# Kernel optimization log

Hardware: AMD Instinct MI355X
Metric: run time of the kernel (lower is better)

The kernel has to match this reference:

```python
import jax, jax.numpy as jnp
import numpy as np

PRE_NMS = 256       # pre_nms_limit default
IOU_THRESH = 0.7    # iou_threshold default
POST_NMS = 128      # post_nms_limit default


def setup_inputs() -> dict:
    key = jax.random.key(0)
    ks = jax.random.split(key, 8)
    B, N, D = 16, 2048, 1024
    feats = jax.random.normal(ks[0], (B, N, D), dtype=jnp.float32)
    # valid boxes in (x1, y1, x2, y2) format
    xy1 = jax.random.uniform(ks[1], (B, N, 2), dtype=jnp.float32) * 1000.0
    wh = jax.random.uniform(ks[2], (B, N, 2), dtype=jnp.float32) * 200.0 + 1.0
    proposals = jnp.concatenate([xy1, xy1 + wh], axis=-1)
    def lin(k, fi, fo):
        return jax.random.normal(k, (fi, fo), dtype=jnp.float32) * (1.0 / np.sqrt(fi))
    Ws1 = lin(ks[3], D, 256); bs1 = jnp.zeros((256,), jnp.float32)
    Ws2 = lin(ks[4], 256, 64); bs2 = jnp.zeros((64,), jnp.float32)
    Wo1 = lin(ks[5], D, 256); bo1 = jnp.zeros((256,), jnp.float32)
    Wo2 = lin(ks[6], 256, 64); bo2 = jnp.zeros((64,), jnp.float32)
    return dict(feats=feats, proposals=proposals, Ws1=Ws1, bs1=bs1, Ws2=Ws2,
                bs2=bs2, Wo1=Wo1, bo1=bo1, Wo2=Wo2, bo2=bo2)


def _nms_keep(boxes, thresh):
    """Greedy NMS; boxes (P,4) already sorted by descending score."""
    P = boxes.shape[0]
    areas = (boxes[:, 2] - boxes[:, 0]) * (boxes[:, 3] - boxes[:, 1])
    lt = jnp.maximum(boxes[:, None, :2], boxes[None, :, :2])
    rb = jnp.minimum(boxes[:, None, 2:], boxes[None, :, 2:])
    wh = jnp.clip(rb - lt, 0.0)
    inter = wh[..., 0] * wh[..., 1]
    iou = inter / (areas[:, None] + areas[None, :] - inter)
    idx = jnp.arange(P)
    def body(i, keep):
        suppress = (iou[i] > thresh) & (idx > i) & keep[i]
        return keep & ~suppress
    return jax.lax.fori_loop(0, P, body, jnp.ones((P,), bool))


def _image_forward(f, boxes, Ws1, bs1, Ws2, bs2, Wo1, bo1, Wo2, bo2):
    # RelPNSimilarity: two small MLPs + sigmoid(subj @ obj^T)
    subj = jax.nn.relu(f @ Ws1 + bs1) @ Ws2 + bs2        # (N, 64)
    obj = jax.nn.relu(f @ Wo1 + bo1) @ Wo2 + bo2         # (N, 64)
    scores = jax.nn.sigmoid(subj @ obj.T)                # (N, N)
    N = f.shape[0]
    # full descending sort + take == top_k; flat index f = i*N + j -> pair (i, j)
    top_scores, top_idx = jax.lax.top_k(scores.reshape(-1), PRE_NMS)
    si = top_idx // N
    oi = top_idx % N
    pairs = jnp.stack([si, oi], axis=1)                  # (PRE_NMS, 2)
    b1 = boxes[si]
    b2 = boxes[oi]
    inter_boxes = jnp.concatenate(
        [jnp.maximum(b1[:, :2], b2[:, :2]), jnp.minimum(b1[:, 2:], b2[:, 2:])],
        axis=1)                                          # (PRE_NMS, 4)
    keep = _nms_keep(inter_boxes, IOU_THRESH)
    # kept indices in score order, padded with non-kept if fewer than POST_NMS
    P = PRE_NMS
    order = jnp.argsort(jnp.where(keep, jnp.arange(P), P + jnp.arange(P)))
    sel = order[:POST_NMS]
    valid = keep[sel]
    out_pairs = jnp.where(valid[:, None], pairs[sel], 0)
    out_scores = jnp.where(valid, top_scores[sel], 0.0)
    out_inter = jnp.where(valid[:, None], inter_boxes[sel], 0.0)
    return out_pairs, out_scores, out_inter, valid


def reference(feats, proposals, Ws1, bs1, Ws2, bs2, Wo1, bo1, Wo2, bo2):
    fn = jax.vmap(_image_forward,
                  in_axes=(0, 0, None, None, None, None, None, None, None, None))
    pairs, scores, inters, valid = fn(feats, proposals, Ws1, bs1, Ws2, bs2,
                                      Wo1, bo1, Wo2, bo2)
    # pairs (B,128,2) int, scores (B,128), inters (B,128,4), valid (B,128) bool
    return pairs, scores, inters, valid
```

## Files before the change

kernel.cpp:

```cpp
#include <hip/hip_runtime.h>
#include <stdint.h>


#define N_PROP 2048
#define D_FEAT 1024
#define H_DIM  256
#define E_DIM  64
#define BATCH  16
#define PRE_NMS 256
#define POST_NMS 128
#define CAND_CAP 32768
#define CNT_STRIDE 64
#define LOGIT_THRESH 11.0f
#define IOU_T 0.7f
#define WT_WHICH (16 * 32 * 512)
#define SO_ELEMS ((size_t)BATCH * 128 * 2 * 512)
#define LBUF_CAP 2048

typedef short sh8 __attribute__((ext_vector_type(8)));
typedef float f4  __attribute__((ext_vector_type(4)));

__device__ inline void decomp3(float f, unsigned& h, unsigned& m, unsigned& l) {
    unsigned u = __float_as_uint(f);
    h = (u + 0x8000u) & 0xFFFF0000u;
    float f1 = f - __uint_as_float(h);
    unsigned u1 = __float_as_uint(f1);
    m = (u1 + 0x8000u) & 0xFFFF0000u;
    float f2 = f1 - __uint_as_float(m);
    l = (__float_as_uint(f2) + 0x8000u) & 0xFFFF0000u;
}

__global__ __launch_bounds__(256) void prep_kernel(
    const float* __restrict__ Ws1, const float* __restrict__ Wo1,
    unsigned short* __restrict__ Wh, unsigned short* __restrict__ Wm,
    unsigned short* __restrict__ Wl)
{
    const int t = threadIdx.x;
    const int nblk = blockIdx.x;
    const int ks = blockIdx.y * 4 + (t >> 6);
    const int which = blockIdx.z;
    const float* W = which ? Wo1 : Ws1;
    const int lane = t & 63;
    const int q = lane >> 4, ln = lane & 15;

    unsigned hb[8], mb[8], lb[8];
#pragma unroll
    for (int j = 0; j < 8; ++j) {
        float v = W[(size_t)(ks * 32 + q * 8 + j) * H_DIM + nblk * 16 + ln];
        decomp3(v, hb[j], mb[j], lb[j]);
    }
    union { unsigned u[4]; sh8 v; } H, M, L;
#pragma unroll
    for (int c = 0; c < 4; ++c) {
        H.u[c] = (hb[2 * c] >> 16) | (hb[2 * c + 1] & 0xFFFF0000u);
        M.u[c] = (mb[2 * c] >> 16) | (mb[2 * c + 1] & 0xFFFF0000u);
        L.u[c] = (lb[2 * c] >> 16) | (lb[2 * c + 1] & 0xFFFF0000u);
    }
    size_t off = ((size_t)which * 16 * 32 + (size_t)nblk * 32 + ks) * 512 + lane * 8;
    *(sh8*)(Wh + off) = H.v;
    *(sh8*)(Wm + off) = M.v;
    *(sh8*)(Wl + off) = L.v;
}

__global__ __launch_bounds__(256) void mlp_fused_kernel(
    const float* __restrict__ feats,
    const unsigned short* __restrict__ Wh, const unsigned short* __restrict__ Wm,
    const unsigned short* __restrict__ Wl,
    const float* __restrict__ bs1,
    const float* __restrict__ Ws2, const float* __restrict__ bs2,
    const float* __restrict__ bo1,
    const float* __restrict__ Wo2, const float* __restrict__ bo2,
    unsigned short* __restrict__ Sh, unsigned short* __restrict__ Sm,
    unsigned short* __restrict__ Sl,
    unsigned short* __restrict__ Oh, unsigned short* __restrict__ Om,
    unsigned short* __restrict__ Ol)
{
    const int t  = threadIdx.x;
    const int rt = blockIdx.x;
    const int b  = blockIdx.y;
    const int r0g = rt * 32;

    __shared__ float lds[4128];
    float* Fs = lds;

    const int lane = t & 63;
    const int l15 = t & 15;
    const int q   = (t >> 4) & 3;
    const int wv  = t >> 6;
    const int wb  = wv * 64;

    f4 acc[2][2][4];
#pragma unroll
    for (int w = 0; w < 2; ++w)
#pragma unroll
        for (int i = 0; i < 2; ++i)
#pragma unroll
            for (int j = 0; j < 4; ++j) acc[w][i][j] = (f4)0.0f;

    const float* fbase = feats + ((size_t)b * N_PROP + r0g) * D_FEAT;
    const int fm = t >> 3, fj = t & 7;

    float4 fpre = *(const float4*)(fbase + (size_t)fm * D_FEAT + fj * 4);

    sh8 nxh[2], nxm[2], nxl[2];
#pragma unroll
    for (int w = 0; w < 2; ++w) {
        size_t off = (size_t)w * WT_WHICH + ((size_t)(wv * 4) * 32) * 512 + lane * 8;
        nxh[w] = *(const sh8*)(Wh + off);
        nxm[w] = *(const sh8*)(Wm + off);
        nxl[w] = *(const sh8*)(Wl + off);
    }

    for (int kt = 0; kt < 32; ++kt) {
        __syncthreads();
        *(float4*)(Fs + fm * 36 + fj * 4) = fpre;
        __syncthreads();
        if (kt + 1 < 32)
            fpre = *(const float4*)(fbase + (size_t)fm * D_FEAT + (kt + 1) * 32 + fj * 4);

        sh8 afh[2], afm[2], afl[2];
#pragma unroll
        for (int mt = 0; mt < 2; ++mt) {
            const float* src = Fs + (mt * 16 + l15) * 36 + q * 8;
            float4 a0 = *(const float4*)(src);
            float4 a1 = *(const float4*)(src + 4);
            float av[8] = {a0.x, a0.y, a0.z, a0.w, a1.x, a1.y, a1.z, a1.w};
            unsigned hb[8], mb[8], lb[8];
#pragma unroll
            for (int e = 0; e < 8; ++e) decomp3(av[e], hb[e], mb[e], lb[e]);
            union { unsigned u[4]; sh8 v; } H, M, L;
#pragma unroll
            for (int c = 0; c < 4; ++c) {
                H.u[c] = (hb[2 * c] >> 16) | (hb[2 * c + 1] & 0xFFFF0000u);
                M.u[c] = (mb[2 * c] >> 16) | (mb[2 * c + 1] & 0xFFFF0000u);
                L.u[c] = (lb[2 * c] >> 16) | (lb[2 * c + 1] & 0xFFFF0000u);
            }
            afh[mt] = H.v; afm[mt] = M.v; afl[mt] = L.v;
        }

#pragma unroll
        for (int nt = 0; nt < 4; ++nt) {
            sh8 cwh[2], cwm[2], cwl[2];
#pragma unroll
            for (int w = 0; w < 2; ++w) {
                cwh[w] = nxh[w]; cwm[w] = nxm[w]; cwl[w] = nxl[w];
            }
            int s = kt * 4 + nt + 1;
            if (s < 128) {
                int knt = s & 3, kkt = s >> 2;
#pragma unroll
                for (int w = 0; w < 2; ++w) {
                    size_t off = (size_t)w * WT_WHICH
                               + ((size_t)(wv * 4 + knt) * 32 + kkt) * 512 + lane * 8;
                    nxh[w] = *(const sh8*)(Wh + off);
                    nxm[w] = *(const sh8*)(Wm + off);
                    nxl[w] = *(const sh8*)(Wl + off);
                }
            }
#pragma unroll
            for (int w = 0; w < 2; ++w)
#pragma unroll
                for (int mt = 0; mt < 2; ++mt) {
                    f4 x = acc[w][mt][nt];
                    x = __builtin_amdgcn_mfma_f32_16x16x32_bf16(afh[mt], cwh[w], x, 0, 0, 0);
                    x = __builtin_amdgcn_mfma_f32_16x16x32_bf16(afh[mt], cwm[w], x, 0, 0, 0);
                    x = __builtin_amdgcn_mfma_f32_16x16x32_bf16(afm[mt], cwh[w], x, 0, 0, 0);
                    x = __builtin_amdgcn_mfma_f32_16x16x32_bf16(afh[mt], cwl[w], x, 0, 0, 0);
                    x = __builtin_amdgcn_mfma_f32_16x16x32_bf16(afm[mt], cwm[w], x, 0, 0, 0);
                    x = __builtin_amdgcn_mfma_f32_16x16x32_bf16(afl[mt], cwh[w], x, 0, 0, 0);
                    acc[w][mt][nt] = x;
                }
        }
    }

    float bc[2][4];
#pragma unroll
    for (int w = 0; w < 2; ++w) {
        const float* B1 = w ? bo1 : bs1;
#pragma unroll
        for (int nt = 0; nt < 4; ++nt) bc[w][nt] = B1[wb + nt * 16 + l15];
    }

    float* Hp  = lds;
    float* W2c = lds + 2080;
    const int tr2 = t >> 4;
    const int tc2 = t & 15;

#pragma unroll
    for (int w = 0; w < 2; ++w) {
        const float* W2 = w ? Wo2 : Ws2;
        const float* B2 = w ? bo2 : bs2;
        unsigned short* Dh = w ? Oh : Sh;
        unsigned short* Dm = w ? Om : Sm;
        unsigned short* Dl = w ? Ol : Sl;

        float acc2[2][4];
#pragma unroll
        for (int i = 0; i < 2; ++i)
#pragma unroll
            for (int j = 0; j < 4; ++j) acc2[i][j] = 0.0f;

        float4 w2pre[2];
#pragma unroll
        for (int i = 0; i < 2; ++i) {
            int lin = (t + i * 256) * 4;
            int row = lin >> 6, col = lin & 63;
            w2pre[i] = *(const float4*)(W2 + (size_t)row * E_DIM + col);
        }

        for (int c = 0; c < 8; ++c) {
            const int p = c >> 1, ch = c & 1;
            __syncthreads();
            if (ch == 0 && wv == p) {
#pragma unroll
                for (int mt = 0; mt < 2; ++mt)
#pragma unroll
                    for (int nt = 0; nt < 4; ++nt)
#pragma unroll
                        for (int r = 0; r < 4; ++r) {
                            float v = acc[w][mt][nt][r] + bc[w][nt];
                            v = v > 0.0f ? v : 0.0f;
                            Hp[(mt * 16 + q * 4 + r) * 65 + nt * 16 + l15] = v;
                        }
            }
#pragma unroll
            for (int i = 0; i < 2; ++i) {
                int lin = (t + i * 256) * 4;
                int row = lin >> 6, col = lin & 63;
                *(float4*)(W2c + row * 64 + col) = w2pre[i];
            }
            if (c + 1 < 8) {
                const int rbase = (c + 1) * 32;
#pragma unroll
                for (int i = 0; i < 2; ++i) {
                    int lin = (t + i * 256) * 4;
                    int row = lin >> 6, col = lin & 63;
                    w2pre[i] = *(const float4*)(W2 + (size_t)(rbase + row) * E_DIM + col);
                }
            }
            __syncthreads();
#pragma unroll 8
            for (int kk = 0; kk < 32; ++kk) {
                int kl = ch * 32 + kk;
                float4 wvv = *(const float4*)(W2c + kk * 64 + tc2 * 4);
                float hv[2];
#pragma unroll
                for (int ri = 0; ri < 2; ++ri) hv[ri] = Hp[(tr2 * 2 + ri) * 65 + kl];
#pragma unroll
                for (int ri = 0; ri < 2; ++ri) {
                    acc2[ri][0] = fmaf(hv[ri], wvv.x, acc2[ri][0]);
                    acc2[ri][1] = fmaf(hv[ri], wvv.y, acc2[ri][1]);
                    acc2[ri][2] = fmaf(hv[ri], wvv.z, acc2[ri][2]);
                    acc2[ri][3] = fmaf(hv[ri], wvv.w, acc2[ri][3]);
                }
            }
        }

        {
            float bb[4] = {B2[tc2 * 4 + 0], B2[tc2 * 4 + 1],
                           B2[tc2 * 4 + 2], B2[tc2 * 4 + 3]};
            const int ks = tc2 >> 3, q2 = (tc2 >> 1) & 3, j0 = (tc2 & 1) * 4;
#pragma unroll
            for (int ri = 0; ri < 2; ++ri) {
                unsigned hb[4], mb[4], lb[4];
#pragma unroll
                for (int ci = 0; ci < 4; ++ci)
                    decomp3(acc2[ri][ci] + bb[ci], hb[ci], mb[ci], lb[ci]);
                int row = r0g + tr2 * 2 + ri;
                int nblk = row >> 4, ln = row & 15;
                size_t so = (((size_t)b * 128 + nblk) * 2 + ks) * 512
                            + (q2 * 16 + ln) * 8 + j0;
                *(uint2*)(Dh + so) = make_uint2((hb[0] >> 16) | (hb[1] & 0xFFFF0000u),
                                                (hb[2] >> 16) | (hb[3] & 0xFFFF0000u));
                *(uint2*)(Dm + so) = make_uint2((mb[0] >> 16) | (mb[1] & 0xFFFF0000u),
                                                (mb[2] >> 16) | (mb[3] & 0xFFFF0000u));
                *(uint2*)(Dl + so) = make_uint2((lb[0] >> 16) | (lb[1] & 0xFFFF0000u),
                                                (lb[2] >> 16) | (lb[3] & 0xFFFF0000u));
            }
        }
    }
}

__global__ __launch_bounds__(256) void score_kernel(
    const unsigned short* __restrict__ Sh, const unsigned short* __restrict__ Sm,
    const unsigned short* __restrict__ Sl,
    const unsigned short* __restrict__ Oh, const unsigned short* __restrict__ Om,
    const unsigned short* __restrict__ Ol,
    unsigned long long* __restrict__ cand, unsigned int* __restrict__ cnt)
{
    const int t = threadIdx.x;
    const int lane = t & 63;
    const int wv = t >> 6;
    const int rt = blockIdx.x >> 1;
    const int half = blockIdx.x & 1;
    const int b = blockIdx.y;
    const int r0g = rt * 64;
    const int ct0 = half * 16, ctEnd = ct0 + 16;
    const int l15 = t & 15;
    const int q   = (t >> 4) & 3;
    const int rh  = wv & 1;
    const int chh = wv >> 1;

    __shared__ unsigned long long lbuf[LBUF_CAP];
    __shared__ unsigned int lcnt, nOut, gbase;
    if (t == 0) lcnt = 0;
    __syncthreads();

    sh8 sfh[2][2], sfm[2][2], sfl[2][2];
#pragma unroll
    for (int mt = 0; mt < 2; ++mt)
#pragma unroll
        for (int ks = 0; ks < 2; ++ks) {
            size_t off = (((size_t)b * 128 + rt * 4 + rh * 2 + mt) * 2 + ks) * 512
                         + lane * 8;
            sfh[mt][ks] = *(const sh8*)(Sh + off);
            sfm[mt][ks] = *(const sh8*)(Sm + off);
            sfl[mt][ks] = *(const sh8*)(Sl + off);
        }

    sh8 oAh[2][2], oAm[2][2], oAl[2][2];
    sh8 oBh[2][2], oBm[2][2], oBl[2][2];

    auto load_o = [&](sh8 (&oh)[2][2], sh8 (&om)[2][2], sh8 (&ol)[2][2], int ct) {
        if (ct < ctEnd) {
#pragma unroll
            for (int nt = 0; nt < 2; ++nt)
#pragma unroll
                for (int ks = 0; ks < 2; ++ks) {
                    size_t off = (((size_t)b * 128 + ct * 4 + chh * 2 + nt) * 2 + ks) * 512
                                 + lane * 8;
                    oh[nt][ks] = *(const sh8*)(Oh + off);
                    om[nt][ks] = *(const sh8*)(Om + off);
                    ol[nt][ks] = *(const sh8*)(Ol + off);
                }
        }
    };

    auto compute = [&](sh8 (&oh)[2][2], sh8 (&om)[2][2], sh8 (&ol)[2][2], int ct) {
        f4 acc[2][2];
#pragma unroll
        for (int mt = 0; mt < 2; ++mt)
#pragma unroll
            for (int nt = 0; nt < 2; ++nt) {
                f4 x = (f4)0.0f;
#pragma unroll
                for (int ks = 0; ks < 2; ++ks) {
                    x = __builtin_amdgcn_mfma_f32_16x16x32_bf16(sfh[mt][ks], oh[nt][ks], x, 0, 0, 0);
                    x = __builtin_amdgcn_mfma_f32_16x16x32_bf16(sfh[mt][ks], om[nt][ks], x, 0, 0, 0);
                    x = __builtin_amdgcn_mfma_f32_16x16x32_bf16(sfm[mt][ks], oh[nt][ks], x, 0, 0, 0);
                    x = __builtin_amdgcn_mfma_f32_16x16x32_bf16(sfh[mt][ks], ol[nt][ks], x, 0, 0, 0);
                    x = __builtin_amdgcn_mfma_f32_16x16x32_bf16(sfm[mt][ks], om[nt][ks], x, 0, 0, 0);
                    x = __builtin_amdgcn_mfma_f32_16x16x32_bf16(sfl[mt][ks], oh[nt][ks], x, 0, 0, 0);
                }
                acc[mt][nt] = x;
            }
#pragma unroll
        for (int mt = 0; mt < 2; ++mt)
#pragma unroll
            for (int nt = 0; nt < 2; ++nt)
#pragma unroll
                for (int r = 0; r < 4; ++r) {
                    float logit = acc[mt][nt][r];
                    if (logit > LOGIT_THRESH) {
                        float score = 1.0f / (1.0f + expf(-logit));
                        unsigned sb = __float_as_uint(score);
                        int row = r0g + rh * 32 + mt * 16 + q * 4 + r;
                        int col = ct * 64 + chh * 32 + nt * 16 + l15;
                        unsigned flat = (unsigned)(row * N_PROP + col);
                        unsigned long long key =
                            ((unsigned long long)sb << 32) | (unsigned)(~flat);
                        unsigned p = atomicAdd(&lcnt, 1u);
                        if (p < LBUF_CAP) lbuf[p] = key;
                    }
                }
    };

    load_o(oAh, oAm, oAl, ct0);
    for (int i = 0; i < 16; i += 2) {
        load_o(oBh, oBm, oBl, ct0 + i + 1);
        compute(oAh, oAm, oAl, ct0 + i);
        load_o(oAh, oAm, oAl, ct0 + i + 2);
        compute(oBh, oBm, oBl, ct0 + i + 1);
    }

    __syncthreads();
    if (t == 0) {
        unsigned n = lcnt > LBUF_CAP ? LBUF_CAP : lcnt;
        nOut = n;
        gbase = n ? atomicAdd(&cnt[(size_t)b * CNT_STRIDE], n) : 0u;
    }
    __syncthreads();
    for (unsigned i = t; i < nOut; i += 256) {
        unsigned pos = gbase + i;
        if (pos < CAND_CAP) cand[(size_t)b * CAND_CAP + pos] = lbuf[i];
    }
}

__device__ inline void bitonic_sort_desc_u64(unsigned long long* a, unsigned n, int t) {
    for (unsigned k = 2; k <= n; k <<= 1)
        for (unsigned j = k >> 1; j > 0; j >>= 1) {
            __syncthreads();
            for (unsigned i = (unsigned)t; i < n; i += 256) {
                unsigned l = i ^ j;
                if (l > i) {
                    unsigned long long x = a[i], y = a[l];
                    bool up = ((i & k) == 0);
                    if (up ? (x < y) : (x > y)) { a[i] = y; a[l] = x; }
                }
            }
        }
    __syncthreads();
}

__global__ __launch_bounds__(256) void select_nms_kernel(
    const unsigned long long* __restrict__ cand, const unsigned int* __restrict__ cnt,
    const float* __restrict__ proposals, float* __restrict__ out)
{
    const int b = blockIdx.x;
    const int t = threadIdx.x;
    const int lane = t & 63;
    const int wv = t >> 6;
    __shared__ unsigned int hist[1024];
    __shared__ unsigned long long selk[256];
    __shared__ unsigned long long pool[4096];
    __shared__ unsigned int nDef, nPool, kc_s, need_s;
    __shared__ float bx1[256], by1[256], bx2[256], by2[256], barea[256];
    __shared__ unsigned int keepf[256];
    __shared__ unsigned int wcnt[4];

    unsigned count = cnt[(size_t)b * CNT_STRIDE];
    if (count > CAND_CAP) count = CAND_CAP;

    for (int i = t; i < 1024; i += 256) hist[i] = 0;
    selk[t] = 0ull;
    if (t == 0) { nDef = 0; nPool = 0; }
    __syncthreads();

    const unsigned long long* cb = cand + (size_t)b * CAND_CAP;
    for (unsigned i = t; i < count; i += 256) {
        unsigned k = 0x3F800000u - (unsigned)(cb[i] >> 32);
        if (k > 1023u) k = 1023u;
        atomicAdd(&hist[k], 1u);
    }
    __syncthreads();
    if (t == 0) {
        unsigned c = 0, kc = 1024, need = 0;
        for (int k = 0; k < 1024; ++k) {
            unsigned prev = c;
            c += hist[k];
            if (c >= PRE_NMS) { kc = (unsigned)k; need = PRE_NMS - prev; break; }
        }
        kc_s = kc; need_s = need;
    }
    __syncthreads();
    const unsigned kc = kc_s, need = need_s;

    for (unsigned i = t; i < count; i += 256) {
        unsigned long long key = cb[i];
        unsigned k = 0x3F800000u - (unsigned)(key >> 32);
        if (k > 1023u) k = 1023u;
        if (k < kc) {
            unsigned p = atomicAdd(&nDef, 1u);
            if (p < 256u) selk[p] = key;
        } else if (k == kc) {
            unsigned p = atomicAdd(&nPool, 1u);
            if (p < 4096u) pool[p] = key;
        }
    }
    __syncthreads();
    unsigned np = nPool; if (np > 4096u) np = 4096u;
    unsigned n2 = 256; while (n2 < np) n2 <<= 1;
    for (unsigned i = t; i < n2; i += 256) if (i >= np) pool[i] = 0ull;
    __syncthreads();
    bitonic_sort_desc_u64(pool, n2, t);

    unsigned nd = nDef; if (nd > 256u) nd = 256u;
    if ((unsigned)t < need && nd + (unsigned)t < 256u) selk[nd + t] = pool[t];
    __syncthreads();
    bitonic_sort_desc_u64(selk, 256u, t);

    float rx1, ry1, rx2, ry2, rar, rscore;
    int rsi, roi;
    {
        unsigned long long key = selk[t];
        unsigned flat = ~(unsigned)(key & 0xFFFFFFFFull);
        unsigned si = (flat >> 11) & 2047u;
        unsigned oi = flat & 2047u;
        rscore = __uint_as_float((unsigned)(key >> 32));
        const float* p1 = proposals + ((size_t)b * N_PROP + si) * 4;
        const float* p2 = proposals + ((size_t)b * N_PROP + oi) * 4;
        rx1 = fmaxf(p1[0], p2[0]);
        ry1 = fmaxf(p1[1], p2[1]);
        rx2 = fminf(p1[2], p2[2]);
        ry2 = fminf(p1[3], p2[3]);
        rar = (rx2 - rx1) * (ry2 - ry1);
        bx1[t] = rx1; by1[t] = ry1; bx2[t] = rx2; by2[t] = ry2; barea[t] = rar;
        rsi = (int)si; roi = (int)oi;
    }
    __syncthreads();

    bool kreg = true;
    for (int w = 0; w < 4; ++w) {
        if (wv == w) {
            for (int l = 0; l < 64; ++l) {
                int   ki  = __shfl((int)kreg, l);
                float ix1 = __shfl(rx1, l);
                float iy1 = __shfl(ry1, l);
                float ix2 = __shfl(rx2, l);
                float iy2 = __shfl(ry2, l);
                float iar = __shfl(rar, l);
                if (ki && lane > l) {
                    float lx = fmaxf(ix1, rx1), ly = fmaxf(iy1, ry1);
                    float rx = fminf(ix2, rx2), ry = fminf(iy2, ry2);
                    float wd = rx - lx; if (wd < 0.0f) wd = 0.0f;
                    float ht = ry - ly; if (ht < 0.0f) ht = 0.0f;
                    float inter = wd * ht;
                    float iou = inter / (iar + rar - inter);
                    if (iou > IOU_T) kreg = false;
                }
            }
            keepf[t] = kreg ? 1u : 0u;
        }
        __syncthreads();
        if (wv > w) {
            for (int l = 0; l < 64; ++l) {
                int i = w * 64 + l;
                if (keepf[i]) {
                    float lx = fmaxf(bx1[i], rx1), ly = fmaxf(by1[i], ry1);
                    float rx = fminf(bx2[i], rx2), ry = fminf(by2[i], ry2);
                    float wd = rx - lx; if (wd < 0.0f) wd = 0.0f;
                    float ht = ry - ly; if (ht < 0.0f) ht = 0.0f;
                    float inter = wd * ht;
                    float iou = inter / (barea[i] + rar - inter);
                    if (iou > IOU_T) kreg = false;
                }
            }
        }
    }
    __syncthreads();

    unsigned long long m = __ballot(kreg);
    unsigned before = __popcll(m & ((1ull << lane) - 1ull));
    if (lane == 0) wcnt[wv] = (unsigned)__popcll(m);
    __syncthreads();
    unsigned base = 0, tot = 0;
#pragma unroll
    for (int w = 0; w < 4; ++w) {
        unsigned c = wcnt[w];
        if (w < wv) base += c;
        tot += c;
    }
    unsigned kb = base + before;
    unsigned pos = kreg ? kb : (tot + (unsigned)t - kb);
    if (pos < POST_NMS) {
        bool valid = kreg;
        float* pairs = out;
        float* scr = out + (size_t)BATCH * POST_NMS * 2;
        float* itb = scr + (size_t)BATCH * POST_NMS;
        float* vld = itb + (size_t)BATCH * POST_NMS * 4;
        size_t s = (size_t)b * POST_NMS + pos;
        pairs[s * 2 + 0] = valid ? (float)rsi : 0.0f;
        pairs[s * 2 + 1] = valid ? (float)roi : 0.0f;
        scr[s] = valid ? rscore : 0.0f;
        itb[s * 4 + 0] = valid ? rx1 : 0.0f;
        itb[s * 4 + 1] = valid ? ry1 : 0.0f;
        itb[s * 4 + 2] = valid ? rx2 : 0.0f;
        itb[s * 4 + 3] = valid ? ry2 : 0.0f;
        vld[s] = valid ? 1.0f : 0.0f;
    }
}

extern "C" void kernel_launch(void* const* d_in, const int* in_sizes, int n_in,
                              void* d_out, int out_size, void* d_ws, size_t ws_size,
                              hipStream_t stream) {
    const float* feats     = (const float*)d_in[0];
    const float* proposals = (const float*)d_in[1];
    const float* Ws1 = (const float*)d_in[2];
    const float* bs1 = (const float*)d_in[3];
    const float* Ws2 = (const float*)d_in[4];
    const float* bs2 = (const float*)d_in[5];
    const float* Wo1 = (const float*)d_in[6];
    const float* bo1 = (const float*)d_in[7];
    const float* Wo2 = (const float*)d_in[8];
    const float* bo2 = (const float*)d_in[9];
    float* out = (float*)d_out;

    char* ws = (char*)d_ws;
    unsigned long long* cand = (unsigned long long*)ws;
    unsigned int* cnt = (unsigned int*)(cand + (size_t)BATCH * CAND_CAP);
    unsigned short* Wth = (unsigned short*)(cnt + BATCH * CNT_STRIDE);
    unsigned short* Wtm = Wth + 2 * WT_WHICH;
    unsigned short* Wtl = Wtm + 2 * WT_WHICH;
    unsigned short* Sh = Wtl + 2 * WT_WHICH;
    unsigned short* Sm = Sh + SO_ELEMS;
    unsigned short* Sl = Sm + SO_ELEMS;
    unsigned short* Oh = Sl + SO_ELEMS;
    unsigned short* Om = Oh + SO_ELEMS;
    unsigned short* Ol = Om + SO_ELEMS;

    hipMemsetAsync(cnt, 0, BATCH * CNT_STRIDE * sizeof(unsigned int), stream);

    prep_kernel<<<dim3(16, 8, 2), 256, 0, stream>>>(Ws1, Wo1, Wth, Wtm, Wtl);
    mlp_fused_kernel<<<dim3(64, BATCH), 256, 0, stream>>>(
        feats, Wth, Wtm, Wtl, bs1, Ws2, bs2, bo1, Wo2, bo2,
        Sh, Sm, Sl, Oh, Om, Ol);
    score_kernel<<<dim3(64, BATCH), 256, 0, stream>>>(
        Sh, Sm, Sl, Oh, Om, Ol, cand, cnt);
    select_nms_kernel<<<BATCH, 256, 0, stream>>>(cand, cnt, proposals, out);
}
```

Before: 592.0 us.

## Split features into bf16 parts once per tile and share object tiles via LDS

Result: slower. 625.6 us (+5.7%).

```diff
diff --git a/kernel.cpp b/kernel.cpp
--- a/kernel.cpp
+++ b/kernel.cpp
@@ -15,7 +15,7 @@
 #define IOU_T 0.7f
 #define WT_WHICH (16 * 32 * 512)
 #define SO_ELEMS ((size_t)BATCH * 128 * 2 * 512)
-#define LBUF_CAP 2048
+#define LBUF_CAP 1920
 
 typedef short sh8 __attribute__((ext_vector_type(8)));
 typedef float f4  __attribute__((ext_vector_type(4)));
@@ -81,14 +81,22 @@
     const int r0g = rt * 32;
 
     __shared__ float lds[4128];
-    float* Fs = lds;
-
-    const int lane = t & 63;
+    unsigned short* fb = (unsigned short*)lds;
+
+    const int hwl = t & 63;
     const int l15 = t & 15;
     const int q   = (t >> 4) & 3;
     const int wv  = t >> 6;
     const int wb  = wv * 64;
 
+    const int dmt = t >> 7;
+    const int dl  = (t >> 1) & 63;
+    const int djh = t & 1;
+    const int drow = dmt * 16 + (dl & 15);
+    const int dk   = (dl >> 4) * 8 + djh * 4;
+    const float* fptr = feats + ((size_t)b * N_PROP + r0g + drow) * D_FEAT + dk;
+    const int dco = dl * 8 + djh * 4;
+
     f4 acc[2][2][4];
 #pragma unroll
     for (int w = 0; w < 2; ++w)
@@ -97,45 +105,45 @@
 #pragma unroll
             for (int j = 0; j < 4; ++j) acc[w][i][j] = (f4)0.0f;
 
-    const float* fbase = feats + ((size_t)b * N_PROP + r0g) * D_FEAT;
-    const int fm = t >> 3, fj = t & 7;
-
-    float4 fpre = *(const float4*)(fbase + (size_t)fm * D_FEAT + fj * 4);
-
     sh8 nxh[2], nxm[2], nxl[2];
 #pragma unroll
     for (int w = 0; w < 2; ++w) {
-        size_t off = (size_t)w * WT_WHICH + ((size_t)(wv * 4) * 32) * 512 + lane * 8;
+        size_t off = (size_t)w * WT_WHICH + ((size_t)(wv * 4) * 32) * 512 + hwl * 8;
         nxh[w] = *(const sh8*)(Wh + off);
         nxm[w] = *(const sh8*)(Wm + off);
         nxl[w] = *(const sh8*)(Wl + off);
     }
 
+    float4 fv = *(const float4*)(fptr);
+
     for (int kt = 0; kt < 32; ++kt) {
+        {
+            float av[4] = {fv.x, fv.y, fv.z, fv.w};
+            unsigned hb[4], mb[4], lb[4];
+#pragma unroll
+            for (int e = 0; e < 4; ++e) decomp3(av[e], hb[e], mb[e], lb[e]);
+            uint2 H = make_uint2((hb[0] >> 16) | (hb[1] & 0xFFFF0000u),
+                                 (hb[2] >> 16) | (hb[3] & 0xFFFF0000u));
+            uint2 M = make_uint2((mb[0] >> 16) | (mb[1] & 0xFFFF0000u),
+                                 (mb[2] >> 16) | (mb[3] & 0xFFFF0000u));
+            uint2 L = make_uint2((lb[0] >> 16) | (lb[1] & 0xFFFF0000u),
+                                 (lb[2] >> 16) | (lb[3] & 0xFFFF0000u));
+            unsigned short* cb = fb + (((kt & 1) * 2 + dmt) * 3) * 512 + dco;
+            *(uint2*)(cb)        = H;
+            *(uint2*)(cb + 512)  = M;
+            *(uint2*)(cb + 1024) = L;
+        }
+        if (kt + 1 < 32)
+            fv = *(const float4*)(fptr + (kt + 1) * 32);
         __syncthreads();
-        *(float4*)(Fs + fm * 36 + fj * 4) = fpre;
-        __syncthreads();
-        if (kt + 1 < 32)
-            fpre = *(const float4*)(fbase + (size_t)fm * D_FEAT + (kt + 1) * 32 + fj * 4);
 
         sh8 afh[2], afm[2], afl[2];
 #pragma unroll
         for (int mt = 0; mt < 2; ++mt) {
-            const float* src = Fs + (mt * 16 + l15) * 36 + q * 8;
-            float4 a0 = *(const float4*)(src);
-            float4 a1 = *(const float4*)(src + 4);
-            float av[8] = {a0.x, a0.y, a0.z, a0.w, a1.x, a1.y, a1.z, a1.w};
-            unsigned hb[8], mb[8], lb[8];
-#pragma unroll
-            for (int e = 0; e < 8; ++e) decomp3(av[e], hb[e], mb[e], lb[e]);
-            union { unsigned u[4]; sh8 v; } H, M, L;
-#pragma unroll
-            for (int c = 0; c < 4; ++c) {
-                H.u[c] = (hb[2 * c] >> 16) | (hb[2 * c + 1] & 0xFFFF0000u);
-                M.u[c] = (mb[2 * c] >> 16) | (mb[2 * c + 1] & 0xFFFF0000u);
-                L.u[c] = (lb[2 * c] >> 16) | (lb[2 * c + 1] & 0xFFFF0000u);
-            }
-            afh[mt] = H.v; afm[mt] = M.v; afl[mt] = L.v;
+            const unsigned short* cb = fb + (((kt & 1) * 2 + mt) * 3) * 512 + hwl * 8;
+            afh[mt] = *(const sh8*)(cb);
+            afm[mt] = *(const sh8*)(cb + 512);
+            afl[mt] = *(const sh8*)(cb + 1024);
         }
 
 #pragma unroll
@@ -151,7 +159,7 @@
 #pragma unroll
                 for (int w = 0; w < 2; ++w) {
                     size_t off = (size_t)w * WT_WHICH
-                               + ((size_t)(wv * 4 + knt) * 32 + kkt) * 512 + lane * 8;
+                               + ((size_t)(wv * 4 + knt) * 32 + kkt) * 512 + hwl * 8;
                     nxh[w] = *(const sh8*)(Wh + off);
                     nxm[w] = *(const sh8*)(Wm + off);
                     nxl[w] = *(const sh8*)(Wl + off);
@@ -289,83 +297,78 @@
     unsigned long long* __restrict__ cand, unsigned int* __restrict__ cnt)
 {
     const int t = threadIdx.x;
-    const int lane = t & 63;
+    const int hwl = t & 63;
     const int wv = t >> 6;
-    const int rt = blockIdx.x >> 1;
-    const int half = blockIdx.x & 1;
+    const int rt = blockIdx.x >> 2;
+    const int cq = blockIdx.x & 3;
     const int b = blockIdx.y;
-    const int r0g = rt * 64;
-    const int ct0 = half * 16, ctEnd = ct0 + 16;
+    const int r0g = rt * 128;
     const int l15 = t & 15;
     const int q   = (t >> 4) & 3;
-    const int rh  = wv & 1;
-    const int chh = wv >> 1;
-
+
+    __shared__ unsigned short oLDS[24 * 512];
     __shared__ unsigned long long lbuf[LBUF_CAP];
     __shared__ unsigned int lcnt, nOut, gbase;
     if (t == 0) lcnt = 0;
-    __syncthreads();
 
     sh8 sfh[2][2], sfm[2][2], sfl[2][2];
 #pragma unroll
     for (int mt = 0; mt < 2; ++mt)
 #pragma unroll
         for (int ks = 0; ks < 2; ++ks) {
-            size_t off = (((size_t)b * 128 + rt * 4 + rh * 2 + mt) * 2 + ks) * 512
-                         + lane * 8;
+            size_t off = (((size_t)b * 128 + rt * 8 + wv * 2 + mt) * 2 + ks) * 512
+                         + hwl * 8;
             sfh[mt][ks] = *(const sh8*)(Sh + off);
             sfm[mt][ks] = *(const sh8*)(Sm + off);
             sfl[mt][ks] = *(const sh8*)(Sl + off);
         }
 
-    sh8 oAh[2][2], oAm[2][2], oAl[2][2];
-    sh8 oBh[2][2], oBm[2][2], oBl[2][2];
-
-    auto load_o = [&](sh8 (&oh)[2][2], sh8 (&om)[2][2], sh8 (&ol)[2][2], int ct) {
-        if (ct < ctEnd) {
-#pragma unroll
-            for (int nt = 0; nt < 2; ++nt)
+    auto ld_stage = [&](sh8 (&st)[6], int ct) {
+#pragma unroll
+        for (int i = 0; i < 6; ++i) {
+            int c = wv * 6 + i;
+            int p = c >> 3, nt = (c >> 1) & 3, ks = c & 1;
+            const unsigned short* P = p == 0 ? Oh : (p == 1 ? Om : Ol);
+            st[i] = *(const sh8*)(P + (((size_t)b * 128 + cq * 32 + ct * 4 + nt) * 2
+                                       + ks) * 512 + hwl * 8);
+        }
+    };
+    auto st_stage = [&](sh8 (&st)[6]) {
+#pragma unroll
+        for (int i = 0; i < 6; ++i)
+            *(sh8*)(oLDS + (wv * 6 + i) * 512 + hwl * 8) = st[i];
+    };
+
+    auto compute = [&](int ct) {
+#pragma unroll
+        for (int nt = 0; nt < 4; ++nt) {
+            sh8 oh[2], om[2], ol[2];
+#pragma unroll
+            for (int ks = 0; ks < 2; ++ks) {
+                oh[ks] = *(const sh8*)(oLDS + (0 * 8 + nt * 2 + ks) * 512 + hwl * 8);
+                om[ks] = *(const sh8*)(oLDS + (1 * 8 + nt * 2 + ks) * 512 + hwl * 8);
+                ol[ks] = *(const sh8*)(oLDS + (2 * 8 + nt * 2 + ks) * 512 + hwl * 8);
+            }
+#pragma unroll
+            for (int mt = 0; mt < 2; ++mt) {
+                f4 x = (f4)0.0f;
 #pragma unroll
                 for (int ks = 0; ks < 2; ++ks) {
-                    size_t off = (((size_t)b * 128 + ct * 4 + chh * 2 + nt) * 2 + ks) * 512
-                                 + lane * 8;
-                    oh[nt][ks] = *(const sh8*)(Oh + off);
-                    om[nt][ks] = *(const sh8*)(Om + off);
-                    ol[nt][ks] = *(const sh8*)(Ol + off);
-                }
-        }
-    };
-
-    auto compute = [&](sh8 (&oh)[2][2], sh8 (&om)[2][2], sh8 (&ol)[2][2], int ct) {
-        f4 acc[2][2];
-#pragma unroll
-        for (int mt = 0; mt < 2; ++mt)
-#pragma unroll
-            for (int nt = 0; nt < 2; ++nt) {
-                f4 x = (f4)0.0f;
-#pragma unroll
-                for (int ks = 0; ks < 2; ++ks) {
-                    x = __builtin_amdgcn_mfma_f32_16x16x32_bf16(sfh[mt][ks], oh[nt][ks], x, 0, 0, 0);
-                    x = __builtin_amdgcn_mfma_f32_16x16x32_bf16(sfh[mt][ks], om[nt][ks], x, 0, 0, 0);
-                    x = __builtin_amdgcn_mfma_f32_16x16x32_bf16(sfm[mt][ks], oh[nt][ks], x, 0, 0, 0);
-                    x = __builtin_amdgcn_mfma_f32_16x16x32_bf16(sfh[mt][ks], ol[nt][ks], x, 0, 0, 0);
-                    x = __builtin_amdgcn_mfma_f32_16x16x32_bf16(sfm[mt][ks], om[nt][ks], x, 0, 0, 0);
-                    x = __builtin_amdgcn_mfma_f32_16x16x32_bf16(sfl[mt][ks], oh[nt][ks], x, 0, 0, 0);
-                }
-                acc[mt][nt] = x;
-            }
-#pragma unroll
-        for (int mt = 0; mt < 2; ++mt)
-#pragma unroll
-            for (int nt = 0; nt < 2; ++nt)
+                    x = __builtin_amdgcn_mfma_f32_16x16x32_bf16(sfh[mt][ks], oh[ks], x, 0, 0, 0);
+                    x = __builtin_amdgcn_mfma_f32_16x16x32_bf16(sfh[mt][ks], om[ks], x, 0, 0, 0);
+                    x = __builtin_amdgcn_mfma_f32_16x16x32_bf16(sfm[mt][ks], oh[ks], x, 0, 0, 0);
+                    x = __builtin_amdgcn_mfma_f32_16x16x32_bf16(sfh[mt][ks], ol[ks], x, 0, 0, 0);
+                    x = __builtin_amdgcn_mfma_f32_16x16x32_bf16(sfm[mt][ks], om[ks], x, 0, 0, 0);
+                    x = __builtin_amdgcn_mfma_f32_16x16x32_bf16(sfl[mt][ks], oh[ks], x, 0, 0, 0);
+                }
 #pragma unroll
                 for (int r = 0; r < 4; ++r) {
-                    float logit = acc[mt][nt][r];
+                    float logit = x[r];
                     if (logit > LOGIT_THRESH) {
                         float score = 1.0f / (1.0f + expf(-logit));
                         unsigned sb = __float_as_uint(score);
-                        int row = r0g + rh * 32 + mt * 16 + q * 4 + r;
-                        int col = ct * 64 + chh * 32 + nt * 16 + l15;
+                        int row = r0g + wv * 32 + mt * 16 + q * 4 + r;
+                        int col = cq * 512 + ct * 64 + nt * 16 + l15;
                         unsigned flat = (unsigned)(row * N_PROP + col);
                         unsigned long long key =
                             ((unsigned long long)sb << 32) | (unsigned)(~flat);
@@ -373,14 +376,23 @@
                         if (p < LBUF_CAP) lbuf[p] = key;
                     }
                 }
+            }
+        }
     };
 
-    load_o(oAh, oAm, oAl, ct0);
-    for (int i = 0; i < 16; i += 2) {
-        load_o(oBh, oBm, oBl, ct0 + i + 1);
-        compute(oAh, oAm, oAl, ct0 + i);
-        load_o(oAh, oAm, oAl, ct0 + i + 2);
-        compute(oBh, oBm, oBl, ct0 + i + 1);
+    sh8 stA[6], stB[6];
+    ld_stage(stA, 0);
+    for (int ci = 0; ci < 8; ci += 2) {
+        ld_stage(stB, ci + 1);
+        __syncthreads();
+        st_stage(stA);
+        __syncthreads();
+        compute(ci);
+        if (ci + 2 < 8) ld_stage(stA, ci + 2);
+        __syncthreads();
+        st_stage(stB);
+        __syncthreads();
+        compute(ci + 1);
     }
 
     __syncthreads();
```
